# Kernel optimization log

Measured on AMD Instinct MI355X. Metric: run time of the kernel, lower is better.

## Reference

```python
import jax, jax.numpy as jnp
import numpy as np

B, T, D = 4, 2048, 2048
H = 16
DH = D // H  # 128
THETA = 10000.0


def _rope(x, offset=0):
    # x: [b, h, t, d]; lucidrains rotary_embedding_torch style (interleaved pairs)
    d = x.shape[-1]
    t = x.shape[-2]
    inv_freq = 1.0 / (THETA ** (jnp.arange(0, d, 2, dtype=jnp.float32) / d))  # [d/2]
    pos = jnp.arange(offset, offset + t, dtype=jnp.float32)
    freqs = pos[:, None] * inv_freq[None, :]              # [t, d/2]
    freqs = jnp.repeat(freqs, 2, axis=-1)                 # [t, d] (n r) interleave
    cos = jnp.cos(freqs).astype(x.dtype)
    sin = jnp.sin(freqs).astype(x.dtype)
    x1 = x[..., 0::2]
    x2 = x[..., 1::2]
    rot = jnp.stack([-x2, x1], axis=-1).reshape(x.shape)  # rotate_half
    return x * cos + rot * sin


def setup_inputs() -> dict:
    key = jax.random.key(0)
    ks = jax.random.split(key, 5)
    s = 1.0 / np.sqrt(D)
    return {
        "x": jax.random.normal(ks[0], (B, T, D), jnp.float32),
        "Wq": jax.random.normal(ks[1], (D, D), jnp.float32) * s,
        "Wk": jax.random.normal(ks[2], (D, D), jnp.float32) * s,
        "Wv": jax.random.normal(ks[3], (D, D), jnp.float32) * s,
        "Wo": jax.random.normal(ks[4], (D, D), jnp.float32) * s,
    }


def reference(x, Wq, Wk, Wv, Wo):
    b, t, d = x.shape
    # QKV projections (bias-free), split heads: b t (h f) -> b h t f
    q = (x @ Wq).reshape(b, t, H, DH).transpose(0, 2, 1, 3)
    k = (x @ Wk).reshape(b, t, H, DH).transpose(0, 2, 1, 3)
    v = (x @ Wv).reshape(b, t, H, DH).transpose(0, 2, 1, 3)
    # rotary embedding on q and k (offset = 0)
    q = _rope(q)
    k = _rope(k)
    # causal scaled dot-product attention
    scale = 1.0 / np.sqrt(DH)
    logits = jnp.einsum('bhtf,bhsf->bhts', q, k) * scale
    causal = jnp.tril(jnp.ones((t, t), dtype=bool))
    logits = jnp.where(causal, logits, jnp.finfo(logits.dtype).min)
    p = jax.nn.softmax(logits, axis=-1)
    y = jnp.einsum('bhts,bhsf->bhtf', p, v)
    # b h t f -> b t (h f), then output projection
    y = y.transpose(0, 2, 1, 3).reshape(b, t, d)
    return y @ Wo
```

## Files before the change

### kernel.cpp

```cpp
#include <hip/hip_runtime.h>
#include <hip/hip_bf16.h>
#include <math.h>

typedef unsigned short u16;
typedef __attribute__((ext_vector_type(8))) __bf16 bf16x8;
typedef __attribute__((ext_vector_type(4))) float f32x4;
typedef __attribute__((ext_vector_type(16))) float f32x16;
typedef __attribute__((ext_vector_type(8))) u16 u16x8;
typedef __attribute__((ext_vector_type(4))) u16 u16x4;
typedef __attribute__((ext_vector_type(4))) unsigned u32x4;

#define T_SEQ 2048
#define DMODEL 2048
#define NH 16
#define DHEAD 128
#define BATCH 4
#define QKV_STR 6144
#define ATTN_SCALE 0.08838834764831845f
#define QSCALE_LOG2E 0.1275411278534803f

#define GLOAD(gp, lp) __builtin_amdgcn_global_load_lds( \
    (const __attribute__((address_space(1))) void*)(gp), \
    (__attribute__((address_space(3))) void*)(lp), 16, 0, 0)

#define BAR() __builtin_amdgcn_s_barrier()
#define LGKM0() do { asm volatile("s_waitcnt lgkmcnt(0)" ::: "memory"); \
                     __builtin_amdgcn_sched_barrier(0); } while (0)
#define VMCNT4() asm volatile("s_waitcnt vmcnt(4)" ::: "memory")
#define MFMA32(A, B, C) __builtin_amdgcn_mfma_f32_32x32x16_bf16(A, B, C, 0, 0, 0)

__device__ __forceinline__ float b2f(u16 u) {
  union { float f; unsigned int i; } x; x.i = ((unsigned int)u) << 16; return x.f;
}
__device__ __forceinline__ u16 f2b(float f) {
  __bf16 h = (__bf16)f;
  return *(u16*)&h;
}
__device__ __forceinline__ unsigned pk2(float lo, float hi2) {
  __bf16 a = (__bf16)lo, b = (__bf16)hi2;
  unsigned short ua = *(unsigned short*)&a, ub = *(unsigned short*)&b;
  return (unsigned)ua | ((unsigned)ub << 16);
}

__global__ __launch_bounds__(256) void cast_f32_bf16(const float* __restrict__ in,
                                                     u16* __restrict__ out) {
  long i = ((long)blockIdx.x * 256 + threadIdx.x) * 8;
  float4 a = *(const float4*)(in + i);
  float4 b = *(const float4*)(in + i + 4);
  u16x8 r;
  r[0] = f2b(a.x); r[1] = f2b(a.y); r[2] = f2b(a.z); r[3] = f2b(a.w);
  r[4] = f2b(b.x); r[5] = f2b(b.y); r[6] = f2b(b.z); r[7] = f2b(b.w);
  *(u16x8*)(out + i) = r;
}

__global__ __launch_bounds__(256) void wtrans_kernel(const float* __restrict__ W,
                                                     u16* __restrict__ Wt) {
  __shared__ float tile[64][65];
  const int k0 = blockIdx.x * 64, n0 = blockIdx.y * 64;
  const int c = threadIdx.x & 63, r4 = threadIdx.x >> 6;
#pragma unroll
  for (int p = 0; p < 16; p++) {
    int r = p * 4 + r4;
    tile[r][c] = W[(long)(k0 + r) * DMODEL + n0 + c];
  }
  __syncthreads();
#pragma unroll
  for (int p = 0; p < 16; p++) {
    int r = p * 4 + r4;
    Wt[(long)(n0 + r) * DMODEL + k0 + c] = f2b(tile[c][r]);
  }
}

__global__ __launch_bounds__(256) void vtrans_kernel(const u16* __restrict__ C,
                                                     u16* __restrict__ Vt) {
  __shared__ u16 tile[64][66];
  const int s0 = blockIdx.x * 64, f0 = blockIdx.y * 64;
  const int bh = blockIdx.z;
  const int b = bh >> 4, h = bh & 15;
  const int c = threadIdx.x & 63, r4 = threadIdx.x >> 6;
#pragma unroll
  for (int p = 0; p < 16; p++) {
    int r = p * 4 + r4;
    tile[r][c] = C[(long)(b * T_SEQ + s0 + r) * QKV_STR + 4096 + h * DHEAD + f0 + c];
  }
  __syncthreads();
#pragma unroll
  for (int p = 0; p < 16; p++) {
    int r = p * 4 + r4;
    Vt[(long)(bh * DHEAD + f0 + r) * T_SEQ + s0 + c] = tile[c][r];
  }
}

__global__ __launch_bounds__(256) void rope_qk_kernel(u16* __restrict__ X) {
  int idx = blockIdx.x * 256 + threadIdx.x;
  int c8 = idx & 511;
  long row = idx >> 9;
  int t = (int)(row & (T_SEQ - 1));
  int i4 = c8 & 15;
  long off = row * QKV_STR + (long)c8 * 8;
  u16x8 v = *(u16x8*)(X + off);
  float o[8];
#pragma unroll
  for (int j = 0; j < 4; j++) {
    int i = i4 * 4 + j;
    float inv = __builtin_amdgcn_exp2f((float)i * -0.20762050593045857f);
    float ang = (float)t * inv;
    float cs = cosf(ang), sn = sinf(ang);
    float x0 = b2f(v[2 * j]), x1 = b2f(v[2 * j + 1]);
    o[2 * j]     = x0 * cs - x1 * sn;
    o[2 * j + 1] = x1 * cs + x0 * sn;
  }
  u16x8 r;
#pragma unroll
  for (int j = 0; j < 8; j++) r[j] = f2b(o[j]);
  *(u16x8*)(X + off) = r;
}

#define LOAD_A(q)                                                      \
  _Pragma("unroll") for (int k = 0; k < 2; k++)                        \
  _Pragma("unroll") for (int m = 0; m < 2; m++) {                      \
    int r = wr * 128 + (q) * 32 + m * 16 + lr;                         \
    int cc = (k * 4 + lc) ^ (r & 7);                                   \
    a[k][m] = *(const bf16x8*)&sA[par][r * 64 + cc * 8];               \
  }

#define LOAD_B()                                                       \
  _Pragma("unroll") for (int k = 0; k < 2; k++)                        \
  _Pragma("unroll") for (int n = 0; n < 4; n++) {                      \
    int r = wc * 64 + n * 16 + lr;                                     \
    int cc = (k * 4 + lc) ^ (r & 7);                                   \
    b[k][n] = *(const bf16x8*)&sB[par][r * 64 + cc * 8];               \
  }

#define MFMA_QUAD(q)                                                   \
  _Pragma("unroll") for (int k = 0; k < 2; k++)                        \
  _Pragma("unroll") for (int n = 0; n < 4; n++)                        \
  _Pragma("unroll") for (int m = 0; m < 2; m++)                        \
    acc[(q) * 2 + m][n] = __builtin_amdgcn_mfma_f32_16x16x32_bf16(     \
        a[k][m], b[k][n], acc[(q) * 2 + m][n], 0, 0, 0);

#define STAGE_HALF(g, ld, ldsp, rc0, t_, h_)                           \
  _Pragma("unroll") for (int j = 0; j < 2; j++) {                      \
    int rl = (h_) * 128 + wid * 16 + j * 8 + (lane >> 3);              \
    int cc = (lane & 7) ^ (lane >> 3);                                 \
    GLOAD((g) + ((rc0) + rl) * (long)(ld) + (long)(t_) * 64 + cc * 8,  \
          (ldsp) + (h_) * 128 * 64 + (wid * 16 + j * 8) * 64);         \
  }

template <int OUT_F32>
__global__ __launch_bounds__(512, 2) void gemm_bt(const u16* __restrict__ A, long lda,
                                                  const u16* __restrict__ Bt,
                                                  void* __restrict__ Cv,
                                                  int M, int N, int K) {
  __shared__ u16 sA[2][256 * 64];
  __shared__ u16 sB[2][256 * 64];
  const int tid = threadIdx.x, lane = tid & 63, wid = tid >> 6;
  const int wr = wid >> 2, wc = wid & 3;
  const int lr = lane & 15, lc = lane >> 4;
  const int id = blockIdx.x;
  const int per = (N >> 8) >> 3;
  const int g8 = id >> 3;
  const long col0 = (long)((id & 7) + 8 * (g8 % per)) * 256;
  const long row0 = (long)(g8 / per) * 256;
  const int NT = K >> 6;

  f32x4 acc[8][4] = {};
  bf16x8 a[2][2], b[2][4];

  STAGE_HALF(Bt, K, &sB[0][0], col0, 0, 0);
  STAGE_HALF(Bt, K, &sB[0][0], col0, 0, 1);
  STAGE_HALF(A, lda, &sA[0][0], row0, 0, 0);
  STAGE_HALF(A, lda, &sA[0][0], row0, 0, 1);
  STAGE_HALF(Bt, K, &sB[1][0], col0, 1, 0);
  STAGE_HALF(Bt, K, &sB[1][0], col0, 1, 1);
  VMCNT4();
  BAR();

  for (int t = 0; t < NT; t++) {
    const int par = t & 1;
    LOAD_B();
    LOAD_A(0);
    if (t + 1 < NT) { STAGE_HALF(A, lda, &sA[par ^ 1][0], row0, t + 1, 0); }
    BAR(); LGKM0();
    __builtin_amdgcn_s_setprio(1); MFMA_QUAD(0); __builtin_amdgcn_s_setprio(0);
    BAR();
    LOAD_A(1);
    if (t + 1 < NT) { STAGE_HALF(A, lda, &sA[par ^ 1][0], row0, t + 1, 1); }
    if (t + 2 < NT) { STAGE_HALF(Bt, K, &sB[par][0], col0, t + 2, 0); }
    BAR(); LGKM0();
    __builtin_amdgcn_s_setprio(1); MFMA_QUAD(1); __builtin_amdgcn_s_setprio(0);
    BAR();
    LOAD_A(2);
    if (t + 2 < NT) { STAGE_HALF(Bt, K, &sB[par][0], col0, t + 2, 1); }
    BAR(); LGKM0();
    __builtin_amdgcn_s_setprio(1); MFMA_QUAD(2); __builtin_amdgcn_s_setprio(0);
    BAR();
    LOAD_A(3);
    VMCNT4();
    BAR(); LGKM0();
    __builtin_amdgcn_s_setprio(1); MFMA_QUAD(3); __builtin_amdgcn_s_setprio(0);
    BAR();
  }

#pragma unroll
  for (int mf = 0; mf < 8; mf++)
#pragma unroll
    for (int n = 0; n < 4; n++)
#pragma unroll
      for (int i = 0; i < 4; i++) {
        long row = row0 + wr * 128 + mf * 16 + lc * 4 + i;
        long col = col0 + wc * 64 + n * 16 + lr;
        float v = acc[mf][n][i];
        if (OUT_F32) ((float*)Cv)[row * N + col] = v;
        else ((u16*)Cv)[row * N + col] = f2b(v);
      }
}

__global__ __launch_bounds__(256, 2) void attn_kernel(const u16* __restrict__ QK,
                                                      const u16* __restrict__ Vt) {
  __shared__ u16 lK[2][64 * 128];
  __shared__ u16 lV[2][128 * 64];
  const int tid = threadIdx.x, lane = tid & 63, w = tid >> 6;
  const int hi = lane >> 5, l31 = lane & 31;
  const int id = blockIdx.x;
  const int qt = 15 - (id >> 6);
  const int bh = id & 63;
  const int b = bh >> 4, h = bh & 15;
  const int qg = qt * 128 + w * 32 + l31;
  const int swz = l31 & 7;

  bf16x8 qf[8];
  const long qrow = (long)(b * T_SEQ + qg) * QKV_STR + h * DHEAD;
#pragma unroll
  for (int kd = 0; kd < 8; kd++) {
    u16x8 raw = *(const u16x8*)(QK + qrow + kd * 16 + hi * 8);
    bf16x8 q;
#pragma unroll
    for (int j = 0; j < 8; j++) q[j] = (__bf16)(b2f(raw[j]) * QSCALE_LOG2E);
    qf[kd] = q;
  }

  f32x16 o0 = {}, o1 = {}, o2 = {}, o3 = {};
  float m_st = -INFINITY, l_st = 0.f;
  const int nt = (qt + 1) * 2;

#define STAGE(nb, kt_)                                                              \
  {                                                                                 \
    _Pragma("unroll")                                                               \
    for (int j = 0; j < 4; j++) {                                                   \
      int sb = (w * 4 + j) * 64;                                                    \
      int slot = sb + lane;                                                         \
      { int r = slot >> 4, pc = slot & 15, cc = pc ^ (r & 7);                       \
        GLOAD(QK + (long)(b * T_SEQ + (kt_) * 64 + r) * QKV_STR + 2048 +            \
                  h * DHEAD + cc * 8,                                               \
              &lK[nb][sb * 8]); }                                                   \
      { int r = slot >> 3, pc = slot & 7, cc = pc ^ (r & 7);                        \
        GLOAD(Vt + (long)(bh * DHEAD + r) * T_SEQ + (kt_) * 64 + cc * 8,            \
              &lV[nb][sb * 8]); }                                                   \
    }                                                                               \
  }

  STAGE(0, 0);
  __syncthreads();

  for (int kt = 0; kt < nt; kt++) {
    const int cur = kt & 1;
    if (kt + 1 < nt) STAGE(cur ^ 1, kt + 1);

    f32x16 st0 = {}, st1 = {};
    __builtin_amdgcn_s_setprio(1);
#pragma unroll
    for (int kd = 0; kd < 8; kd++) {
      int pc = (kd * 2 + hi) ^ swz;
      bf16x8 kf0 = *(const bf16x8*)&lK[cur][l31 * 128 + pc * 8];
      bf16x8 kf1 = *(const bf16x8*)&lK[cur][(32 + l31) * 128 + pc * 8];
      st0 = MFMA32(kf0, qf[kd], st0);
      st1 = MFMA32(kf1, qf[kd], st1);
    }
    __builtin_amdgcn_s_setprio(0);

    if (kt * 64 + 63 > qt * 128 + w * 32) {
#pragma unroll
      for (int r = 0; r < 16; r++) {
        int sl = kt * 64 + (r & 3) + 8 * (r >> 2) + 4 * hi;
        if (sl > qg) st0[r] = -1e30f;
        if (sl + 32 > qg) st1[r] = -1e30f;
      }
    }

    float mx = -1e30f;
#pragma unroll
    for (int r = 0; r < 16; r++) mx = fmaxf(mx, fmaxf(st0[r], st1[r]));
    mx = fmaxf(mx, __shfl_xor(mx, 32, 64));
    if (__any(mx > m_st + 8.0f)) {
      float mnew = fmaxf(m_st, mx);
      float corr = __builtin_amdgcn_exp2f(m_st - mnew);
      m_st = mnew;
      l_st *= corr;
#pragma unroll
      for (int r = 0; r < 16; r++) {
        o0[r] *= corr; o1[r] *= corr; o2[r] *= corr; o3[r] *= corr;
      }
    }
    float rs = 0.f;
#pragma unroll
    for (int r = 0; r < 16; r++) {
      st0[r] = __builtin_amdgcn_exp2f(st0[r] - m_st); rs += st0[r];
      st1[r] = __builtin_amdgcn_exp2f(st1[r] - m_st); rs += st1[r];
    }
    l_st += rs + __shfl_xor(rs, 32, 64);

    __builtin_amdgcn_s_setprio(1);
#define PVHALF(stX, sb)                                                        \
    _Pragma("unroll")                                                          \
    for (int g = 0; g < 2; g++) {                                              \
      unsigned A0 = pk2(stX[8 * g + 0], stX[8 * g + 1]);                       \
      unsigned A1 = pk2(stX[8 * g + 2], stX[8 * g + 3]);                       \
      unsigned B0 = pk2(stX[8 * g + 4], stX[8 * g + 5]);                       \
      unsigned B1 = pk2(stX[8 * g + 6], stX[8 * g + 7]);                       \
      unsigned xA0 = __shfl_xor(A0, 32, 64);                                   \
      unsigned xA1 = __shfl_xor(A1, 32, 64);                                   \
      unsigned xB0 = __shfl_xor(B0, 32, 64);                                   \
      unsigned xB1 = __shfl_xor(B1, 32, 64);                                   \
      u32x4 pw;                                                                \
      pw[0] = hi ? xB0 : A0;                                                   \
      pw[1] = hi ? xB1 : A1;                                                   \
      pw[2] = hi ? B0 : xA0;                                                   \
      pw[3] = hi ? B1 : xA1;                                                   \
      bf16x8 pa = *(bf16x8*)&pw;                                               \
      const int ks = (sb) * 2 + g;                                             \
      int pc0 = (ks * 2 + hi) ^ swz;                                           \
      bf16x8 vb0 = *(const bf16x8*)&lV[cur][(l31) * 64 + pc0 * 8];             \
      o0 = MFMA32(vb0, pa, o0);                                                \
      bf16x8 vb1 = *(const bf16x8*)&lV[cur][(32 + l31) * 64 + pc0 * 8];        \
      o1 = MFMA32(vb1, pa, o1);                                                \
      bf16x8 vb2 = *(const bf16x8*)&lV[cur][(64 + l31) * 64 + pc0 * 8];        \
      o2 = MFMA32(vb2, pa, o2);                                                \
      bf16x8 vb3 = *(const bf16x8*)&lV[cur][(96 + l31) * 64 + pc0 * 8];        \
      o3 = MFMA32(vb3, pa, o3);                                                \
    }
    PVHALF(st0, 0)
    PVHALF(st1, 1)
#undef PVHALF
    __builtin_amdgcn_s_setprio(0);

    __syncthreads();
  }

  float inv = __builtin_amdgcn_rcpf(l_st);
#define WR(oN, n)                                                              \
  _Pragma("unroll")                                                            \
  for (int rq = 0; rq < 4; rq++) {                                             \
    u16x4 pk;                                                                  \
    _Pragma("unroll")                                                          \
    for (int j = 0; j < 4; j++) pk[j] = f2b(oN[rq * 4 + j] * inv);             \
    *(u16x4*)((u16*)QK + qrow + 4096 + (n) * 32 + rq * 8 + hi * 4) = pk;       \
  }
  WR(o0, 0) WR(o1, 1) WR(o2, 2) WR(o3, 3)
#undef WR
#undef STAGE
}

extern "C" void kernel_launch(void* const* d_in, const int* in_sizes, int n_in,
                              void* d_out, int out_size, void* d_ws, size_t ws_size,
                              hipStream_t stream) {
  const float* x  = (const float*)d_in[0];
  const float* Wq = (const float*)d_in[1];
  const float* Wk = (const float*)d_in[2];
  const float* Wv = (const float*)d_in[3];
  const float* Wo = (const float*)d_in[4];
  float* out = (float*)d_out;
  char* ws = (char*)d_ws;

  const long MB = 1048576L;
  u16* xb   = (u16*)(ws);
  u16* Wqt  = (u16*)(ws + 32 * MB);
  u16* Wkt  = (u16*)(ws + 40 * MB);
  u16* Wvt  = (u16*)(ws + 48 * MB);
  u16* Wot  = (u16*)(ws + 56 * MB);
  u16* Cqkv = (u16*)(ws + 64 * MB);
  u16* Vtb  = xb;

  cast_f32_bf16<<<8192, 256, 0, stream>>>(x, xb);
  dim3 wt_g(32, 32);
  wtrans_kernel<<<wt_g, 256, 0, stream>>>(Wq, Wqt);
  wtrans_kernel<<<wt_g, 256, 0, stream>>>(Wk, Wkt);
  wtrans_kernel<<<wt_g, 256, 0, stream>>>(Wv, Wvt);
  wtrans_kernel<<<wt_g, 256, 0, stream>>>(Wo, Wot);

  gemm_bt<0><<<768, 512, 0, stream>>>(xb, 2048, Wqt, Cqkv, 8192, 6144, 2048);

  rope_qk_kernel<<<16384, 256, 0, stream>>>(Cqkv);

  dim3 vt_g(32, 2, 64);
  vtrans_kernel<<<vt_g, 256, 0, stream>>>(Cqkv, Vtb);

  attn_kernel<<<1024, 256, 0, stream>>>(Cqkv, Vtb);

  gemm_bt<1><<<256, 512, 0, stream>>>(Cqkv + 4096, QKV_STR, Wot, (void*)out,
                                      8192, 2048, 2048);
}
```

Before: 451.8 us.

## Merge weight transposes into one launch, unroll GEMM loop, relax LDS wait barrier

The four weight transpose launches become one launch whose z grid dimension selects the weight and its output slot, which saves launch overhead and lets the blocks share the device. Separately, the GEMM main loop is unrolled by two, and the sched_barrier that followed each lgkmcnt wait is removed so the compiler can schedule around it. Dropping the scheduling fence may let the compiler reorder instructions in ways that hurt the hand-tuned MFMA/LDS interleave, and the unroll raises register pressure.

After: 444.6 us. About the same (-1.6%).

```diff
diff --git a/kernel.cpp b/kernel.cpp
--- a/kernel.cpp
+++ b/kernel.cpp
@@ -24,8 +24,7 @@
     (__attribute__((address_space(3))) void*)(lp), 16, 0, 0)
 
 #define BAR() __builtin_amdgcn_s_barrier()
-#define LGKM0() do { asm volatile("s_waitcnt lgkmcnt(0)" ::: "memory"); \
-                     __builtin_amdgcn_sched_barrier(0); } while (0)
+#define LGKM0() asm volatile("s_waitcnt lgkmcnt(0)" ::: "memory")
 #define VMCNT4() asm volatile("s_waitcnt vmcnt(4)" ::: "memory")
 #define MFMA32(A, B, C) __builtin_amdgcn_mfma_f32_32x32x16_bf16(A, B, C, 0, 0, 0)
 
@@ -53,9 +52,15 @@
   *(u16x8*)(out + i) = r;
 }
 
-__global__ __launch_bounds__(256) void wtrans_kernel(const float* __restrict__ W,
-                                                     u16* __restrict__ Wt) {
+__global__ __launch_bounds__(256) void wtrans4_kernel(const float* __restrict__ W0,
+                                                      const float* __restrict__ W1,
+                                                      const float* __restrict__ W2,
+                                                      const float* __restrict__ W3,
+                                                      u16* __restrict__ WtBase) {
   __shared__ float tile[64][65];
+  const int z = blockIdx.z;
+  const float* W = (z == 0) ? W0 : (z == 1) ? W1 : (z == 2) ? W2 : W3;
+  u16* Wt = WtBase + (long)z * 4194304;
   const int k0 = blockIdx.x * 64, n0 = blockIdx.y * 64;
   const int c = threadIdx.x & 63, r4 = threadIdx.x >> 6;
 #pragma unroll
@@ -176,6 +181,7 @@
   VMCNT4();
   BAR();
 
+#pragma unroll 2
   for (int t = 0; t < NT; t++) {
     const int par = t & 1;
     LOAD_B();
@@ -374,21 +380,15 @@
 
   const long MB = 1048576L;
   u16* xb   = (u16*)(ws);
-  u16* Wqt  = (u16*)(ws + 32 * MB);
-  u16* Wkt  = (u16*)(ws + 40 * MB);
-  u16* Wvt  = (u16*)(ws + 48 * MB);
-  u16* Wot  = (u16*)(ws + 56 * MB);
+  u16* Wt4  = (u16*)(ws + 32 * MB);
   u16* Cqkv = (u16*)(ws + 64 * MB);
   u16* Vtb  = xb;
 
   cast_f32_bf16<<<8192, 256, 0, stream>>>(x, xb);
-  dim3 wt_g(32, 32);
-  wtrans_kernel<<<wt_g, 256, 0, stream>>>(Wq, Wqt);
-  wtrans_kernel<<<wt_g, 256, 0, stream>>>(Wk, Wkt);
-  wtrans_kernel<<<wt_g, 256, 0, stream>>>(Wv, Wvt);
-  wtrans_kernel<<<wt_g, 256, 0, stream>>>(Wo, Wot);
-
-  gemm_bt<0><<<768, 512, 0, stream>>>(xb, 2048, Wqt, Cqkv, 8192, 6144, 2048);
+  dim3 wt_g(32, 32, 4);
+  wtrans4_kernel<<<wt_g, 256, 0, stream>>>(Wq, Wk, Wv, Wo, Wt4);
+
+  gemm_bt<0><<<768, 512, 0, stream>>>(xb, 2048, Wt4, Cqkv, 8192, 6144, 2048);
 
   rope_qk_kernel<<<16384, 256, 0, stream>>>(Cqkv);
 
@@ -397,6 +397,6 @@
 
   attn_kernel<<<1024, 256, 0, stream>>>(Cqkv, Vtb);
 
-  gemm_bt<1><<<256, 512, 0, stream>>>(Cqkv + 4096, QKV_STR, Wot, (void*)out,
-                                      8192, 2048, 2048);
-}
+  gemm_bt<1><<<256, 512, 0, stream>>>(Cqkv + 4096, QKV_STR, Wt4 + 3 * 4194304L,
+                                      (void*)out, 8192, 2048, 2048);
+}
```
